# Kernel optimization log

Hardware: AMD Instinct MI355X
Metric: run time of the kernel (lower is better)

Reference implementation:

```python
import jax, jax.numpy as jnp
import numpy as np

B, S, MEM, L, E, H = 8, 512, 512, 4, 512, 8
DH = E // H
OBS = 128
K = MEM + S


def setup_inputs() -> dict:
    key = jax.random.key(0)
    ks = jax.random.split(key, 16)
    def w(k, shape, s=0.02):
        return jax.random.normal(k, shape, jnp.float32) * s
    # causal-with-memory mask: query i may attend to kv positions j <= MEM + i
    mask = jnp.arange(K)[None, None, None, :] <= (MEM + jnp.arange(S))[None, None, :, None]
    return {
        "obs": w(ks[0], (B, S, OBS), 1.0),
        "memories": w(ks[1], (B, MEM, L, E), 1.0),
        "mask": mask,
        "W_enc": w(ks[2], (OBS, E)), "b_enc": jnp.zeros((E,), jnp.float32),
        "ln1_s": jnp.ones((L, E), jnp.float32), "ln1_b": jnp.zeros((L, E), jnp.float32),
        "Wq": w(ks[3], (L, E, H, DH)), "bq": jnp.zeros((L, H, DH), jnp.float32),
        "Wk": w(ks[4], (L, E, H, DH)), "bk": jnp.zeros((L, H, DH), jnp.float32),
        "Wv": w(ks[5], (L, E, H, DH)), "bv": jnp.zeros((L, H, DH), jnp.float32),
        "Wr": w(ks[6], (L, E, H, DH)),
        "u_bias": w(ks[7], (L, H, DH)), "v_bias": w(ks[8], (L, H, DH)),
        "Wo": w(ks[9], (L, H, DH, E)), "bo": jnp.zeros((L, E), jnp.float32),
        "ln2_s": jnp.ones((L, E), jnp.float32), "ln2_b": jnp.zeros((L, E), jnp.float32),
        "W1": w(ks[10], (L, E, E)), "b1": jnp.zeros((L, E), jnp.float32),
        "W2": w(ks[11], (L, E, E)), "b2": jnp.zeros((L, E), jnp.float32),
    }


def _ln(x, s, b, eps=1e-6):
    m = x.mean(-1, keepdims=True)
    v = ((x - m) ** 2).mean(-1, keepdims=True)
    return (x - m) * jax.lax.rsqrt(v + eps) * s + b


def _rel_shift(x):
    # Transformer-XL relative shift: [B,H,Q,Kk] -> shifted [B,H,Q,Kk]
    b, h, q, k = x.shape
    x = jnp.pad(x, ((0, 0), (0, 0), (0, 0), (1, 0)))
    return x.reshape(b, h, k + 1, q)[:, :, 1:, :].reshape(b, h, q, k)


def _forward(obs, memories, mask, W_enc, b_enc, ln1_s, ln1_b, Wq, bq, Wk, bk, Wv, bv,
             Wr, u_bias, v_bias, Wo, bo, ln2_s, ln2_b, W1, b1, W2, b2):
    x = obs @ W_enc + b_enc  # [B,S,E]
    klen = memories.shape[1] + x.shape[1]
    e = x.shape[-1]
    # PositionalEmbedding: pos_seq = [klen, klen-1, ..., 1]
    inv_freq = 1.0 / (10000.0 ** (jnp.arange(0, e, 2, dtype=jnp.float32) / e))
    sin_inp = jnp.outer(jnp.arange(klen, 0, -1, dtype=jnp.float32), inv_freq)
    pe = jnp.concatenate([jnp.sin(sin_inp), jnp.cos(sin_inp)], axis=-1)  # [K,E]
    scale = 1.0 / jnp.sqrt(jnp.asarray(Wq.shape[-1], jnp.float32))
    for i in range(Wq.shape[0]):
        mem_cat = jnp.concatenate([memories[:, :, i], x], axis=1)  # [B,K,E]
        vk = _ln(mem_cat, ln1_s[i], ln1_b[i])
        qn = _ln(x, ln1_s[i], ln1_b[i])
        q = jnp.einsum('bse,ehd->bshd', qn, Wq[i]) + bq[i]
        k = jnp.einsum('bke,ehd->bkhd', vk, Wk[i]) + bk[i]
        vv = jnp.einsum('bke,ehd->bkhd', vk, Wv[i]) + bv[i]
        r = jnp.einsum('ke,ehd->khd', pe, Wr[i])
        ac = jnp.einsum('bqhd,bkhd->bhqk', q + u_bias[i], k)     # content term
        bd = _rel_shift(jnp.einsum('bqhd,khd->bhqk', q + v_bias[i], r))  # position term
        scores = jnp.where(mask, (ac + bd) * scale, jnp.float32(-1e30))
        attn = jax.nn.softmax(scores, axis=-1)
        o = jnp.einsum('bhqk,bkhd->bqhd', attn, vv)
        attn_out = jnp.einsum('bqhd,hde->bqe', o, Wo[i]) + bo[i]
        h = x + attn_out                      # residual (gating=False)
        hn = _ln(h, ln2_s[i], ln2_b[i])
        ff = jax.nn.gelu(hn @ W1[i] + b1[i]) @ W2[i] + b2[i]
        x = ff + h
    return x


def reference(obs, memories, mask, W_enc, b_enc, ln1_s, ln1_b, Wq, bq, Wk, bk, Wv, bv,
              Wr, u_bias, v_bias, Wo, bo, ln2_s, ln2_b, W1, b1, W2, b2):
    return _forward(obs, memories, mask, W_enc, b_enc, ln1_s, ln1_b, Wq, bq, Wk, bk,
                    Wv, bv, Wr, u_bias, v_bias, Wo, bo, ln2_s, ln2_b, W1, b1, W2, b2)
```

## Files before the change

kernel.cpp:

```cpp
#include <hip/hip_runtime.h>
#include <hip/hip_bf16.h>
#include <math.h>

#define B     8
#define S     512
#define MEM   512
#define L     4
#define E     512
#define H     8
#define DH    64
#define OBS   128
#define KLEN  1024
#define FQ    64
#define FK    64

typedef __hip_bfloat16 bf16;
using frag_ab = __attribute__((ext_vector_type(8))) short;
using frag_cd = __attribute__((ext_vector_type(4))) float;

__device__ __forceinline__ float gelu_tanh(float x) {
    return 0.5f * x * (1.0f + tanhf(0.7978845608028654f * (x + 0.044715f * x * x * x)));
}
__device__ __forceinline__ unsigned short f2bs(float x) {
    bf16 h = __float2bfloat16(x); return *(unsigned short*)&h;
}
__device__ __forceinline__ float bs2f(short s) {
    union { unsigned u; float f; } t; t.u = ((unsigned)(unsigned short)s) << 16; return t.f;
}

__global__ __launch_bounds__(256) void setup_kernel(
    const float* __restrict__ obs, bf16* __restrict__ obsb, bf16* __restrict__ pe)
{
    const int i = blockIdx.x * 256 + threadIdx.x;
    if (i < B * S * OBS) {
        obsb[i] = __float2bfloat16(obs[i]);
    } else {
        const int idx = i - B * S * OBS;
        const int p = idx >> 9;
        const int j = idx & 511;
        const float pos = (float)(KLEN - p);
        const int m = (j < 256) ? j : (j - 256);
        const float invf = expf(-(float)(2 * m) * (9.210340371976184f / (float)E));
        const float a = pos * invf;
        pe[idx] = __float2bfloat16((j < 256) ? sinf(a) : cosf(a));
    }
}

__global__ __launch_bounds__(256) void transpose_all_kernel(
    const float* __restrict__ Wq, const float* __restrict__ Wk,
    const float* __restrict__ Wv, const float* __restrict__ Wr,
    const float* __restrict__ Wo, const float* __restrict__ W1,
    const float* __restrict__ W2, const float* __restrict__ Wenc,
    bf16* __restrict__ WqT, bf16* __restrict__ WkvT, bf16* __restrict__ WrT,
    bf16* __restrict__ WoT, bf16* __restrict__ W1T, bf16* __restrict__ W2T,
    bf16* __restrict__ WencT)
{
    __shared__ float t[32][33];
    const int z = blockIdx.z;
    const int bn = blockIdx.x * 32, bk = blockIdx.y * 32;
    const int tx = threadIdx.x & 31, ty = threadIdx.x >> 5;
    if (z == 28) {
        if (blockIdx.y >= OBS / 32) return;
        #pragma unroll
        for (int r = 0; r < 32; r += 8)
            t[ty + r][tx] = Wenc[(size_t)(bk + ty + r) * E + bn + tx];
        __syncthreads();
        #pragma unroll
        for (int r = 0; r < 32; r += 8)
            WencT[(size_t)(bn + ty + r) * OBS + bk + tx] = __float2bfloat16(t[tx][ty + r]);
        return;
    }
    const int which = z >> 2, li = z & 3;
    const size_t so = (size_t)li * E * E;
    const float* src; bf16* dst;
    switch (which) {
        case 0: src = Wq + so; dst = WqT + so; break;
        case 1: src = Wk + so; dst = WkvT + (size_t)li * 2 * E * E; break;
        case 2: src = Wv + so; dst = WkvT + (size_t)li * 2 * E * E + (size_t)E * E; break;
        case 3: src = Wr + so; dst = WrT + so; break;
        case 4: src = Wo + so; dst = WoT + so; break;
        case 5: src = W1 + so; dst = W1T + so; break;
        default: src = W2 + so; dst = W2T + so; break;
    }
    #pragma unroll
    for (int r = 0; r < 32; r += 8)
        t[ty + r][tx] = src[(size_t)(bk + ty + r) * E + bn + tx];
    __syncthreads();
    #pragma unroll
    for (int r = 0; r < 32; r += 8)
        dst[(size_t)(bn + ty + r) * E + bk + tx] = __float2bfloat16(t[tx][ty + r]);
}

__device__ __forceinline__ void gemm_body(
    short* As, short* Bs,
    const bf16* __restrict__ A, const bf16* __restrict__ Bt,
    int m0, int n0, int K, int N,
    const float* bias, const float* bias_u, const float* bias_v,
    const float* res, float* Cf, bf16* Cb, bf16* Cb2, int act, int mode)
{
    const int tid = threadIdx.x;
    const int w = tid >> 6, lane = tid & 63;
    const int wm2 = (w >> 1) * 64, wn2 = (w & 1) * 32;
    const int fr = lane & 15, quad = lane >> 4;

    const int arow = tid >> 1, acol = (tid & 1) * 32;
    const int brow = tid >> 2, bcol = (tid & 3) * 16;
    const short* Ag = (const short*)A + (size_t)(m0 + arow) * K + acol;
    const short* Bg = (const short*)Bt + (size_t)(n0 + brow) * K + bcol;
    short* Asw = &As[arow * 72 + acol];
    short* Bsw = &Bs[brow * 72 + bcol];

    frag_cd acc[4][2];
    #pragma unroll
    for (int i = 0; i < 4; ++i)
        #pragma unroll
        for (int j = 0; j < 2; ++j)
            acc[i][j] = (frag_cd)(0.0f);

    uint4 a0 = *(const uint4*)(Ag);
    uint4 a1 = *(const uint4*)(Ag + 8);
    uint4 a2 = *(const uint4*)(Ag + 16);
    uint4 a3 = *(const uint4*)(Ag + 24);
    uint4 b0 = *(const uint4*)(Bg);
    uint4 b1 = *(const uint4*)(Bg + 8);

    for (int k0 = 0; k0 < K; k0 += 64) {
        __syncthreads();
        *(uint4*)(Asw) = a0; *(uint4*)(Asw + 8) = a1;
        *(uint4*)(Asw + 16) = a2; *(uint4*)(Asw + 24) = a3;
        *(uint4*)(Bsw) = b0; *(uint4*)(Bsw + 8) = b1;
        if (k0 + 64 < K) {
            a0 = *(const uint4*)(Ag + k0 + 64);
            a1 = *(const uint4*)(Ag + k0 + 72);
            a2 = *(const uint4*)(Ag + k0 + 80);
            a3 = *(const uint4*)(Ag + k0 + 88);
            b0 = *(const uint4*)(Bg + k0 + 64);
            b1 = *(const uint4*)(Bg + k0 + 72);
        }
        asm volatile("s_waitcnt lgkmcnt(0)" ::: "memory");
        __builtin_amdgcn_s_barrier();
        __builtin_amdgcn_sched_barrier(0);
        #pragma unroll
        for (int kh = 0; kh < 2; ++kh) {
            frag_ab af[4], bfr[2];
            #pragma unroll
            for (int i = 0; i < 4; ++i)
                af[i] = *(const frag_ab*)&As[(wm2 + i * 16 + fr) * 72 + kh * 32 + quad * 8];
            #pragma unroll
            for (int j = 0; j < 2; ++j)
                bfr[j] = *(const frag_ab*)&Bs[(wn2 + j * 16 + fr) * 72 + kh * 32 + quad * 8];
            #pragma unroll
            for (int i = 0; i < 4; ++i)
                #pragma unroll
                for (int j = 0; j < 2; ++j)
                    acc[i][j] = __builtin_amdgcn_mfma_f32_16x16x32_bf16(af[i], bfr[j], acc[i][j], 0, 0, 0);
        }
    }

    if (mode == 2 && n0 >= 512) {
        short* ts = As;
        __syncthreads();
        #pragma unroll
        for (int i = 0; i < 4; ++i) {
            #pragma unroll
            for (int r = 0; r < 4; ++r) {
                const int kl = wm2 + i * 16 + quad * 4 + r;
                #pragma unroll
                for (int j = 0; j < 2; ++j) {
                    const int dl = wn2 + j * 16 + fr;
                    ts[dl * 130 + kl] =
                        (short)f2bs(acc[i][j][r] + bias_v[(n0 - 512) + dl]);
                }
            }
        }
        __syncthreads();
        const int bb = m0 >> 10;
        const int kb = m0 & 1023;
        const int dl = tid >> 2;
        const int q4 = tid & 3;
        short vals[32];
        #pragma unroll
        for (int i2 = 0; i2 < 32; ++i2) {
            const int kp  = q4 * 32 + i2;
            const int kpl = kp & 63;
            const int src = (kp & 64) + (((kpl & 3) << 4) | (kpl >> 2));
            vals[i2] = ts[dl * 130 + src];
        }
        short* dst = (short*)Cb2 + ((size_t)(bb * E + (n0 - 512) + dl)) * KLEN
                   + kb + q4 * 32;
        *(uint4*)(dst)      = *(const uint4*)&vals[0];
        *(uint4*)(dst + 8)  = *(const uint4*)&vals[8];
        *(uint4*)(dst + 16) = *(const uint4*)&vals[16];
        *(uint4*)(dst + 24) = *(const uint4*)&vals[24];
        return;
    }

    #pragma unroll
    for (int i = 0; i < 4; ++i) {
        #pragma unroll
        for (int r = 0; r < 4; ++r) {
            const int m = m0 + wm2 + i * 16 + quad * 4 + r;
            #pragma unroll
            for (int j = 0; j < 2; ++j) {
                const int n = n0 + wn2 + j * 16 + fr;
                float v = acc[i][j][r];
                if (bias) v += bias[n];
                if (act)  v = gelu_tanh(v);
                if (res)  v += res[(size_t)m * N + n];
                if (mode == 2) {
                    Cb[(size_t)m * 512 + n] = __float2bfloat16(v + bias_u[n]);
                } else if (mode == 1) {
                    Cb[(size_t)m * N + n]  = __float2bfloat16((v + bias_u[n]) * 0.125f);
                    Cb2[(size_t)m * N + n] = __float2bfloat16((v + bias_v[n]) * 0.125f);
                } else {
                    if (Cf) Cf[(size_t)m * N + n] = v;
                    if (Cb) Cb[(size_t)m * N + n] = __float2bfloat16(v);
                }
            }
        }
    }
}

__device__ __forceinline__ void gemm64_body(
    short* As, short* Bs,
    const bf16* __restrict__ A, const bf16* __restrict__ Bt,
    int m0, int n0, int K, int N,
    const float* bias, const float* res, float* Cf, bf16* Cb, int act,
    float* stats)
{
    const int tid = threadIdx.x;
    const int w = tid >> 6, lane = tid & 63;
    const int wm2 = (w >> 1) * 32, wn2 = (w & 1) * 32;
    const int fr = lane & 15, quad = lane >> 4;

    const int arow = tid >> 2, acol = (tid & 3) * 16;
    const short* Ag = (const short*)A + (size_t)(m0 + arow) * K + acol;
    const short* Bg = (const short*)Bt + (size_t)(n0 + arow) * K + acol;
    short* Asw = &As[arow * 72 + acol];
    short* Bsw = &Bs[arow * 72 + acol];

    frag_cd acc[2][2];
    #pragma unroll
    for (int i = 0; i < 2; ++i)
        #pragma unroll
        for (int j = 0; j < 2; ++j)
            acc[i][j] = (frag_cd)(0.0f);

    uint4 a0 = *(const uint4*)(Ag);
    uint4 a1 = *(const uint4*)(Ag + 8);
    uint4 b0 = *(const uint4*)(Bg);
    uint4 b1 = *(const uint4*)(Bg + 8);

    for (int k0 = 0; k0 < K; k0 += 64) {
        __syncthreads();
        *(uint4*)(Asw) = a0; *(uint4*)(Asw + 8) = a1;
        *(uint4*)(Bsw) = b0; *(uint4*)(Bsw + 8) = b1;
        if (k0 + 64 < K) {
            a0 = *(const uint4*)(Ag + k0 + 64);
            a1 = *(const uint4*)(Ag + k0 + 72);
            b0 = *(const uint4*)(Bg + k0 + 64);
            b1 = *(const uint4*)(Bg + k0 + 72);
        }
        asm volatile("s_waitcnt lgkmcnt(0)" ::: "memory");
        __builtin_amdgcn_s_barrier();
        __builtin_amdgcn_sched_barrier(0);
        #pragma unroll
        for (int kh = 0; kh < 2; ++kh) {
            frag_ab af[2], bfr[2];
            #pragma unroll
            for (int i = 0; i < 2; ++i)
                af[i] = *(const frag_ab*)&As[(wm2 + i * 16 + fr) * 72 + kh * 32 + quad * 8];
            #pragma unroll
            for (int j = 0; j < 2; ++j)
                bfr[j] = *(const frag_ab*)&Bs[(wn2 + j * 16 + fr) * 72 + kh * 32 + quad * 8];
            #pragma unroll
            for (int i = 0; i < 2; ++i)
                #pragma unroll
                for (int j = 0; j < 2; ++j)
                    acc[i][j] = __builtin_amdgcn_mfma_f32_16x16x32_bf16(af[i], bfr[j], acc[i][j], 0, 0, 0);
        }
    }

    #pragma unroll
    for (int i = 0; i < 2; ++i) {
        #pragma unroll
        for (int r = 0; r < 4; ++r) {
            const int m = m0 + wm2 + i * 16 + quad * 4 + r;
            float s = 0.0f, sq = 0.0f;
            #pragma unroll
            for (int j = 0; j < 2; ++j) {
                const int n = n0 + wn2 + j * 16 + fr;
                float v = acc[i][j][r];
                if (bias) v += bias[n];
                if (act)  v = gelu_tanh(v);
                if (res)  v += res[(size_t)m * N + n];
                if (Cf) Cf[(size_t)m * N + n] = v;
                if (Cb) Cb[(size_t)m * N + n] = __float2bfloat16(v);
                s += v; sq = fmaf(v, v, sq);
            }
            if (stats) {
                s  += __shfl_xor(s, 1, 64);  sq += __shfl_xor(sq, 1, 64);
                s  += __shfl_xor(s, 2, 64);  sq += __shfl_xor(sq, 2, 64);
                s  += __shfl_xor(s, 4, 64);  sq += __shfl_xor(sq, 4, 64);
                s  += __shfl_xor(s, 8, 64);  sq += __shfl_xor(sq, 8, 64);
                if (fr == 0) {
                    atomicAdd(&stats[2 * m], s);
                    atomicAdd(&stats[2 * m + 1], sq);
                }
            }
        }
    }
}

__global__ __launch_bounds__(256) void mfma_gemm_kernel(
    const bf16* __restrict__ A, const bf16* __restrict__ Bt,
    const float* __restrict__ bias, const float* __restrict__ res,
    float* __restrict__ Cf, bf16* __restrict__ Cb,
    int K, int N, int act, float* stats)
{
    __shared__ short As[64 * 72];
    __shared__ short Bs[64 * 72];
    const int pid = blockIdx.x;
    const int swz = ((pid & 7) << 6) | (pid >> 3);
    gemm64_body(As, Bs, A, Bt, (swz >> 3) * 64, (swz & 7) * 64, K, N,
                bias, res, Cf, Cb, act, stats);
}

__global__ __launch_bounds__(256) void mfma_gemm_ln_kernel(
    const float* __restrict__ A, const bf16* __restrict__ Bt,
    const float* __restrict__ ST,
    const float* __restrict__ gam, const float* __restrict__ bet,
    const float* __restrict__ bias, bf16* __restrict__ Cb)
{
    __shared__ short As[64 * 72];
    __shared__ short Bs[64 * 72];
    __shared__ float gls[E], bls[E];
    const int pid = blockIdx.x;
    const int swz = ((pid & 7) << 6) | (pid >> 3);
    const int m0 = (swz >> 3) * 64, n0 = (swz & 7) * 64;
    const int tid = threadIdx.x;
    *(float2*)&gls[tid * 2] = *(const float2*)&gam[tid * 2];
    *(float2*)&bls[tid * 2] = *(const float2*)&bet[tid * 2];

    const int w = tid >> 6, lane = tid & 63;
    const int wm2 = (w >> 1) * 32, wn2 = (w & 1) * 32;
    const int fr = lane & 15, quad = lane >> 4;

    const int arow = tid >> 2, acol = (tid & 3) * 16;
    const int g = m0 + arow;
    const float mean = ST[2 * g] * (1.0f / E);
    const float var  = ST[2 * g + 1] * (1.0f / E) - mean * mean;
    const float rstd = rsqrtf(var + 1e-6f);
    const float* Agf = A + (size_t)g * E + acol;
    const short* Bg = (const short*)Bt + (size_t)(n0 + arow) * E + acol;
    short* Asw = &As[arow * 72 + acol];
    short* Bsw = &Bs[arow * 72 + acol];

    frag_cd acc[2][2];
    #pragma unroll
    for (int i = 0; i < 2; ++i)
        #pragma unroll
        for (int j = 0; j < 2; ++j)
            acc[i][j] = (frag_cd)(0.0f);

    float4 f0 = *(const float4*)(Agf);
    float4 f1 = *(const float4*)(Agf + 4);
    float4 f2 = *(const float4*)(Agf + 8);
    float4 f3 = *(const float4*)(Agf + 12);
    uint4 b0 = *(const uint4*)(Bg);
    uint4 b1 = *(const uint4*)(Bg + 8);

    for (int k0 = 0; k0 < E; k0 += 64) {
        __syncthreads();
        {
            const float* gp = &gls[k0 + acol];
            const float* bp = &bls[k0 + acol];
            union { uint4 u; unsigned short s[8]; } p0, p1;
            p0.s[0] = f2bs((f0.x - mean) * rstd * gp[0]  + bp[0]);
            p0.s[1] = f2bs((f0.y - mean) * rstd * gp[1]  + bp[1]);
            p0.s[2] = f2bs((f0.z - mean) * rstd * gp[2]  + bp[2]);
            p0.s[3] = f2bs((f0.w - mean) * rstd * gp[3]  + bp[3]);
            p0.s[4] = f2bs((f1.x - mean) * rstd * gp[4]  + bp[4]);
            p0.s[5] = f2bs((f1.y - mean) * rstd * gp[5]  + bp[5]);
            p0.s[6] = f2bs((f1.z - mean) * rstd * gp[6]  + bp[6]);
            p0.s[7] = f2bs((f1.w - mean) * rstd * gp[7]  + bp[7]);
            p1.s[0] = f2bs((f2.x - mean) * rstd * gp[8]  + bp[8]);
            p1.s[1] = f2bs((f2.y - mean) * rstd * gp[9]  + bp[9]);
            p1.s[2] = f2bs((f2.z - mean) * rstd * gp[10] + bp[10]);
            p1.s[3] = f2bs((f2.w - mean) * rstd * gp[11] + bp[11]);
            p1.s[4] = f2bs((f3.x - mean) * rstd * gp[12] + bp[12]);
            p1.s[5] = f2bs((f3.y - mean) * rstd * gp[13] + bp[13]);
            p1.s[6] = f2bs((f3.z - mean) * rstd * gp[14] + bp[14]);
            p1.s[7] = f2bs((f3.w - mean) * rstd * gp[15] + bp[15]);
            *(uint4*)(Asw) = p0.u; *(uint4*)(Asw + 8) = p1.u;
        }
        *(uint4*)(Bsw) = b0; *(uint4*)(Bsw + 8) = b1;
        if (k0 + 64 < E) {
            f0 = *(const float4*)(Agf + k0 + 64);
            f1 = *(const float4*)(Agf + k0 + 68);
            f2 = *(const float4*)(Agf + k0 + 72);
            f3 = *(const float4*)(Agf + k0 + 76);
            b0 = *(const uint4*)(Bg + k0 + 64);
            b1 = *(const uint4*)(Bg + k0 + 72);
        }
        asm volatile("s_waitcnt lgkmcnt(0)" ::: "memory");
        __builtin_amdgcn_s_barrier();
        __builtin_amdgcn_sched_barrier(0);
        #pragma unroll
        for (int kh = 0; kh < 2; ++kh) {
            frag_ab af[2], bfr[2];
            #pragma unroll
            for (int i = 0; i < 2; ++i)
                af[i] = *(const frag_ab*)&As[(wm2 + i * 16 + fr) * 72 + kh * 32 + quad * 8];
            #pragma unroll
            for (int j = 0; j < 2; ++j)
                bfr[j] = *(const frag_ab*)&Bs[(wn2 + j * 16 + fr) * 72 + kh * 32 + quad * 8];
            #pragma unroll
            for (int i = 0; i < 2; ++i)
                #pragma unroll
                for (int j = 0; j < 2; ++j)
                    acc[i][j] = __builtin_amdgcn_mfma_f32_16x16x32_bf16(af[i], bfr[j], acc[i][j], 0, 0, 0);
        }
    }

    #pragma unroll
    for (int i = 0; i < 2; ++i) {
        #pragma unroll
        for (int r = 0; r < 4; ++r) {
            const int m = m0 + wm2 + i * 16 + quad * 4 + r;
            #pragma unroll
            for (int j = 0; j < 2; ++j) {
                const int n = n0 + wn2 + j * 16 + fr;
                const float v = gelu_tanh(acc[i][j][r] + bias[n]);
                Cb[(size_t)m * E + n] = __float2bfloat16(v);
            }
        }
    }
}

__global__ __launch_bounds__(256) void qkvr_kernel(
    const bf16* __restrict__ QN, const bf16* __restrict__ VK,
    const bf16* __restrict__ PE_, const bf16* __restrict__ WqT,
    const bf16* __restrict__ WkvT, const bf16* __restrict__ WrT,
    const float* __restrict__ bq, const float* __restrict__ ub,
    const float* __restrict__ vbias, const float* __restrict__ bk,
    const float* __restrict__ bv,
    bf16* __restrict__ QU, bf16* __restrict__ QV,
    bf16* __restrict__ KB, bf16* __restrict__ VT, bf16* __restrict__ RB)
{
    __shared__ short As[128 * 72];
    __shared__ short Bs[64 * 72];
    const int bid = blockIdx.x;
    if (bid < 256) {
        const int swz = ((bid & 7) << 5) | (bid >> 3);
        gemm_body(As, Bs, QN, WqT, (swz >> 3) * 128, (swz & 7) * 64, E, E,
                  bq, ub, vbias, nullptr, nullptr, QU, QV, 0, 1);
    } else if (bid < 1280) {
        const int id = bid - 256;
        const int swz = ((id & 7) << 7) | (id >> 3);
        gemm_body(As, Bs, VK, WkvT, (swz >> 4) * 128, (swz & 15) * 64, E, 2 * E,
                  nullptr, bk, bv, nullptr, nullptr, KB, VT, 0, 2);
    } else {
        const int id = bid - 1280;
        const int swz = ((id & 7) << 3) | (id >> 3);
        gemm_body(As, Bs, PE_, WrT, (swz >> 3) * 128, (swz & 7) * 64, E, E,
                  nullptr, nullptr, nullptr, nullptr, nullptr, RB, nullptr, 0, 0);
    }
}

__global__ __launch_bounds__(256) void ln1_kernel(
    const float* __restrict__ mem, const float* __restrict__ X, int li,
    const float* __restrict__ gam, const float* __restrict__ bet,
    bf16* __restrict__ qn, bf16* __restrict__ vkdst, float* __restrict__ st)
{
    const int blk = blockIdx.x;
    const int t = threadIdx.x;
    if (blk < 32) st[blk * 256 + t] = 0.0f;
    const bool isMem = blk < B * MEM;
    const int rr = isMem ? blk : (blk - B * MEM);
    const float* sp = isMem ? (mem + ((size_t)rr * L + li) * E)
                            : (X + (size_t)rr * E);
    const float x0 = sp[t], x1 = sp[t + 256];
    float s = x0 + x1, ss = fmaf(x0, x0, x1 * x1);
    #pragma unroll
    for (int off = 32; off; off >>= 1) { s += __shfl_down(s, off, 64); ss += __shfl_down(ss, off, 64); }
    __shared__ float tmp[8];
    const int wid = t >> 6, lane = t & 63;
    if (!lane) { tmp[wid] = s; tmp[4 + wid] = ss; }
    __syncthreads();
    s = tmp[0] + tmp[1] + tmp[2] + tmp[3];
    ss = tmp[4] + tmp[5] + tmp[6] + tmp[7];
    const float mean = s * (1.0f / E);
    const float var = ss * (1.0f / E) - mean * mean;
    const float rstd = rsqrtf(var + 1e-6f);
    const float y0 = (x0 - mean) * rstd * gam[t] + bet[t];
    const float y1 = (x1 - mean) * rstd * gam[t + 256] + bet[t + 256];
    const int b = rr >> 9, p = rr & 511;
    if (isMem) {
        bf16* dst = vkdst + ((size_t)b * KLEN + p) * E;
        dst[t] = __float2bfloat16(y0); dst[t + 256] = __float2bfloat16(y1);
    } else {
        qn[(size_t)rr * E + t]       = __float2bfloat16(y0);
        qn[(size_t)rr * E + t + 256] = __float2bfloat16(y1);
        bf16* d2 = vkdst + ((size_t)b * KLEN + MEM + p) * E;
        d2[t] = __float2bfloat16(y0); d2[t + 256] = __float2bfloat16(y1);
    }
}

__global__ __launch_bounds__(256) void mfma_flash_kernel(
    const bf16* __restrict__ Qu,
    const bf16* __restrict__ Qv,
    const bf16* __restrict__ Kb,
    const bf16* __restrict__ Vt,
    const bf16* __restrict__ Rb,
    bf16* __restrict__ O)
{
    const int pid = blockIdx.x;
    const int swz = ((pid & 7) << 6) | (pid >> 3);
    const int qphys = swz & 7;
    const int hb = swz >> 3;
    const int h = hb & 7, b = hb >> 3;
    const int qt = (qphys & 1) ? (7 - (qphys >> 1)) : (qphys >> 1);
    const int q0 = qt * FQ;
    const int t = threadIdx.x;
    const int w = t >> 6, lane = t & 63;
    const int fr = lane & 15, quad = lane >> 4;
    const int qbase = q0 + w * 16;

    __shared__ short Ks[64 * 64];
    __shared__ short Vs[64 * 64];
    __shared__ short Rs[128 * 64];
    __shared__ short BDs[4 * 80 * 18];
    __shared__ short Ps[4 * 16 * 64];

    const int fxk = fr & 7;
    const int xq0 = (quad ^ fxk) << 3;
    const int xq1 = ((quad + 4) ^ fxk) << 3;

    const short* quptr = (const short*)Qu + ((size_t)(b * S + qbase + fr)) * E + h * DH + quad * 8;
    const frag_ab au0 = *(const frag_ab*)(quptr);
    const frag_ab au1 = *(const frag_ab*)(quptr + 32);
    const short* qvptr = (const short*)Qv + ((size_t)(b * S + qbase + fr)) * E + h * DH + quad * 8;
    const frag_ab av0 = *(const frag_ab*)(qvptr);
    const frag_ab av1 = *(const frag_ab*)(qvptr + 32);

    frag_cd accO[4];
    #pragma unroll
    for (int i = 0; i < 4; ++i) accO[i] = (frag_cd)(0.0f);
    float mrow[4] = {-3.0e38f, -3.0e38f, -3.0e38f, -3.0e38f};
    float lrow[4] = {0.f, 0.f, 0.f, 0.f};

    const int srow = t >> 2, scol = (t & 3) * 16;
    const short* kg = (const short*)Kb + ((size_t)(b * KLEN + srow)) * E + h * DH + scol;
    const short* vg = (const short*)Vt + ((size_t)(b * E + h * DH + srow)) * KLEN + scol;
    const int sxs = srow & 7;
    const int scb = (t & 3) * 2;
    const int kvw0 = (srow << 6) + (((scb    ) ^ sxs) << 3);
    const int kvw1 = (srow << 6) + (((scb + 1) ^ sxs) << 3);
    const int ntb0 = 3 - w;
    const int b0 = 448 - q0;

    {
        const int rr = t >> 1, rc = (t & 1) * 32;
        const int j = b0 + rr;
        const int slot = j & 127;
        const int sx = slot & 7, cb = rc >> 3;
        const short* rp = (const short*)Rb + (size_t)j * E + h * DH + rc;
        *(uint4*)&Rs[(slot << 6) + (((cb    ) ^ sx) << 3)] = *(const uint4*)(rp);
        *(uint4*)&Rs[(slot << 6) + (((cb + 1) ^ sx) << 3)] = *(const uint4*)(rp + 8);
        *(uint4*)&Rs[(slot << 6) + (((cb + 2) ^ sx) << 3)] = *(const uint4*)(rp + 16);
        *(uint4*)&Rs[(slot << 6) + (((cb + 3) ^ sx) << 3)] = *(const uint4*)(rp + 24);
    }

    const int ntiles = 9 + qt;

    const int r64 = t >> 2, rc4 = (t & 3) * 16;
    uint4 ka0, ka1, va0, va1, ra0, ra1;
    int rslot = 0;
    {
        ka0 = *(const uint4*)(kg);
        ka1 = *(const uint4*)(kg + 8);
        va0 = *(const uint4*)(vg);
        va1 = *(const uint4*)(vg + 8);
    }

    for (int kt = 0; kt < ntiles; ++kt) {
        const int k0 = kt * FK;
        __syncthreads();
        {
            *(uint4*)&Ks[kvw0] = ka0;
            *(uint4*)&Ks[kvw1] = ka1;
            *(uint4*)&Vs[kvw0] = va0;
            *(uint4*)&Vs[kvw1] = va1;
        }
        if (kt >= 1) {
            const int sx = rslot & 7;
            *(uint4*)&Rs[(rslot << 6) + (((scb    ) ^ sx) << 3)] = ra0;
            *(uint4*)&Rs[(rslot << 6) + (((scb + 1) ^ sx) << 3)] = ra1;
        }
        if (kt + 1 < ntiles) {
            const short* kp = kg + (size_t)(k0 + FK) * E;
            ka0 = *(const uint4*)(kp);
            ka1 = *(const uint4*)(kp + 8);
            const short* vp = vg + k0 + FK;
            va0 = *(const uint4*)(vp);
            va1 = *(const uint4*)(vp + 8);
            int j = b0 + 64 * (kt + 1) + 64 + r64;
            rslot = j & 127;
            if (j > KLEN - 1) j = KLEN - 1;
            const short* rp = (const short*)Rb + (size_t)j * E + h * DH + rc4;
            ra0 = *(const uint4*)(rp);
            ra1 = *(const uint4*)(rp + 8);
        }
        asm volatile("s_waitcnt lgkmcnt(0)" ::: "memory");
        __builtin_amdgcn_s_barrier();
        __builtin_amdgcn_sched_barrier(0);

        const int roff = (b0 + 64 * kt) & 127;

        __builtin_amdgcn_s_setprio(1);
        #pragma unroll
        for (int i = 0; i < 5; ++i) {
            const int ntb = ntb0 + i;
            const int slot = (roff + ntb * 16 + fr) & 127;
            const frag_ab rf0 = *(const frag_ab*)&Rs[(slot << 6) + xq0];
            const frag_ab rf1 = *(const frag_ab*)&Rs[(slot << 6) + xq1];
            frag_cd z = (frag_cd)(0.0f);
            z = __builtin_amdgcn_mfma_f32_16x16x32_bf16(av0, rf0, z, 0, 0, 0);
            z = __builtin_amdgcn_mfma_f32_16x16x32_bf16(av1, rf1, z, 0, 0, 0);
            union { unsigned u[2]; unsigned short sh[4]; } pk;
            pk.sh[0] = f2bs(z[0]); pk.sh[1] = f2bs(z[1]);
            pk.sh[2] = f2bs(z[2]); pk.sh[3] = f2bs(z[3]);
            const int bdw = (w * 80 + i * 16 + fr) * 18 + quad * 4;
            *(unsigned*)&BDs[bdw]     = pk.u[0];
            *(unsigned*)&BDs[bdw + 2] = pk.u[1];
        }

        frag_cd sc[4];
        #pragma unroll
        for (int nt = 0; nt < 4; ++nt) {
            const int krow = (nt * 16 + fr) << 6;
            const frag_ab kf0 = *(const frag_ab*)&Ks[krow + xq0];
            const frag_ab kf1 = *(const frag_ab*)&Ks[krow + xq1];
            frag_cd z = (frag_cd)(0.0f);
            z = __builtin_amdgcn_mfma_f32_16x16x32_bf16(au0, kf0, z, 0, 0, 0);
            z = __builtin_amdgcn_mfma_f32_16x16x32_bf16(au1, kf1, z, 0, 0, 0);
            sc[nt] = z;
        }
        __builtin_amdgcn_s_setprio(0);

        const bool edge = (kt == ntiles - 1);
        #pragma unroll
        for (int r = 0; r < 4; ++r) {
            const int qw = quad * 4 + r;
            float sv[4];
            #pragma unroll
            for (int nt = 0; nt < 4; ++nt) {
                const int jlr = nt * 16 + fr + 15 - qw;
                const float bd = bs2f(BDs[(w * 80 + jlr) * 18 + qw]);
                sv[nt] = sc[nt][r] + bd;
            }
            if (edge) {
                const int qrow = qbase + qw;
                #pragma unroll
                for (int nt = 0; nt < 4; ++nt)
                    if (k0 + nt * 16 + fr > MEM + qrow) sv[nt] = -1e30f;
            }
            const float locmax = fmaxf(fmaxf(sv[0], sv[1]), fmaxf(sv[2], sv[3]));
            if (__any(locmax > mrow[r] + 4.0f)) {
                float tm = locmax;
                tm = fmaxf(tm, __shfl_xor(tm, 1, 64));
                tm = fmaxf(tm, __shfl_xor(tm, 2, 64));
                tm = fmaxf(tm, __shfl_xor(tm, 4, 64));
                tm = fmaxf(tm, __shfl_xor(tm, 8, 64));
                const float mn = fmaxf(mrow[r], tm);
                const float al = __expf(mrow[r] - mn);
                lrow[r] *= al;
                #pragma unroll
                for (int nt = 0; nt < 4; ++nt) accO[nt][r] *= al;
                mrow[r] = mn;
            }
            const float p0 = __expf(sv[0] - mrow[r]), p1 = __expf(sv[1] - mrow[r]);
            const float p2 = __expf(sv[2] - mrow[r]), p3 = __expf(sv[3] - mrow[r]);
            lrow[r] += (p0 + p1) + (p2 + p3);
            union { uint2 u2; unsigned short sh[4]; } pq;
            pq.sh[0] = f2bs(p0); pq.sh[1] = f2bs(p1);
            pq.sh[2] = f2bs(p2); pq.sh[3] = f2bs(p3);
            const int pw = (w << 10) + (qw << 6)
                         + (((fr >> 1) ^ (qw & 7)) << 3) + ((fr & 1) << 2);
            *(uint2*)&Ps[pw] = pq.u2;
        }

        const frag_ab pf0 = *(const frag_ab*)&Ps[(w << 10) + (fr << 6) + xq0];
        const frag_ab pf1 = *(const frag_ab*)&Ps[(w << 10) + (fr << 6) + xq1];
        __builtin_amdgcn_s_setprio(1);
        #pragma unroll
        for (int nt = 0; nt < 4; ++nt) {
            const int vrow = (nt * 16 + fr) << 6;
            const frag_ab vf0 = *(const frag_ab*)&Vs[vrow + xq0];
            const frag_ab vf1 = *(const frag_ab*)&Vs[vrow + xq1];
            accO[nt] = __builtin_amdgcn_mfma_f32_16x16x32_bf16(pf0, vf0, accO[nt], 0, 0, 0);
            accO[nt] = __builtin_amdgcn_mfma_f32_16x16x32_bf16(pf1, vf1, accO[nt], 0, 0, 0);
        }
        __builtin_amdgcn_s_setprio(0);
    }

    #pragma unroll
    for (int r = 0; r < 4; ++r) {
        float lsum = lrow[r];
        lsum += __shfl_xor(lsum, 1, 64);
        lsum += __shfl_xor(lsum, 2, 64);
        lsum += __shfl_xor(lsum, 4, 64);
        lsum += __shfl_xor(lsum, 8, 64);
        const float inv = 1.0f / lsum;
        bf16* po = O + ((size_t)(b * S + qbase + quad * 4 + r)) * E + h * DH + fr;
        #pragma unroll
        for (int nt = 0; nt < 4; ++nt)
            po[nt * 16] = __float2bfloat16(accO[nt][r] * inv);
    }
}

extern "C" void kernel_launch(void* const* d_in, const int* in_sizes, int n_in,
                              void* d_out, int out_size, void* d_ws, size_t ws_size,
                              hipStream_t stream)
{
    const float* obs  = (const float*)d_in[0];
    const float* mem  = (const float*)d_in[1];
    const float* Wenc = (const float*)d_in[3];
    const float* benc = (const float*)d_in[4];
    const float* ln1s = (const float*)d_in[5];
    const float* ln1b = (const float*)d_in[6];
    const float* Wq   = (const float*)d_in[7];
    const float* bq   = (const float*)d_in[8];
    const float* Wk   = (const float*)d_in[9];
    const float* bk   = (const float*)d_in[10];
    const float* Wv   = (const float*)d_in[11];
    const float* bv   = (const float*)d_in[12];
    const float* Wr   = (const float*)d_in[13];
    const float* ub   = (const float*)d_in[14];
    const float* vb   = (const float*)d_in[15];
    const float* Wo   = (const float*)d_in[16];
    const float* bo   = (const float*)d_in[17];
    const float* ln2s = (const float*)d_in[18];
    const float* ln2b = (const float*)d_in[19];
    const float* W1   = (const float*)d_in[20];
    const float* b1   = (const float*)d_in[21];
    const float* W2   = (const float*)d_in[22];
    const float* b2   = (const float*)d_in[23];

    float* wsf = (float*)d_ws;
    float* X = wsf;
    bf16* wsb = (bf16*)(wsf + (size_t)B * S * E);
    size_t ob = 0;
    bf16* OBSb = wsb + ob; ob += (size_t)B * S * OBS;
    bf16* QNb  = wsb + ob; ob += (size_t)B * S * E;
    bf16* PEb  = wsb + ob; ob += (size_t)KLEN * E;
    bf16* RBb  = wsb + ob; ob += (size_t)KLEN * E;
    bf16* WencT= wsb + ob; ob += (size_t)OBS * E;
    bf16* WqT  = wsb + ob; ob += (size_t)L * E * E;
    bf16* WkvT = wsb + ob; ob += (size_t)L * 2 * E * E;
    bf16* WrT  = wsb + ob; ob += (size_t)L * E * E;
    bf16* WoT  = wsb + ob; ob += (size_t)L * E * E;
    bf16* W1T  = wsb + ob; ob += (size_t)L * E * E;
    bf16* W2T  = wsb + ob; ob += (size_t)L * E * E;
    bf16* QUb  = wsb + ob; ob += (size_t)B * S * E;
    bf16* QVb  = wsb + ob; ob += (size_t)B * S * E;
    bf16* KBb  = wsb + ob; ob += (size_t)B * KLEN * E;
    bf16* VTb  = wsb + ob; ob += (size_t)B * E * KLEN;
    bf16* OBb  = wsb + ob; ob += (size_t)B * S * E;
    float* ST  = (float*)(wsb + ob); ob += 16384;
    char* uni = (char*)(wsb + ob);
    bf16*  VKb = (bf16*)uni;
    float* HB  = (float*)uni;
    bf16*  FFb = (bf16*)(uni + ((size_t)8 << 20));


    transpose_all_kernel<<<dim3(E / 32, E / 32, 29), 256, 0, stream>>>(
        Wq, Wk, Wv, Wr, Wo, W1, W2, Wenc, WqT, WkvT, WrT, WoT, W1T, W2T, WencT);
    setup_kernel<<<(B * S * OBS + KLEN * E) / 256, 256, 0, stream>>>(obs, OBSb, PEb);

    mfma_gemm_kernel<<<512, 256, 0, stream>>>(
        OBSb, WencT, benc, nullptr, X, nullptr, OBS, E, 0, nullptr);

    for (int li = 0; li < L; ++li) {
        const size_t wOff = (size_t)li * E * E;
        const size_t vOff = (size_t)li * E;

        ln1_kernel<<<2 * B * S, 256, 0, stream>>>(
            mem, X, li, ln1s + vOff, ln1b + vOff, QNb, VKb, ST);

        qkvr_kernel<<<1344, 256, 0, stream>>>(
            QNb, VKb, PEb, WqT + wOff, WkvT + (size_t)li * 2 * E * E, WrT + wOff,
            bq + vOff, ub + vOff, vb + vOff, bk + vOff, bv + vOff,
            QUb, QVb, KBb, VTb, RBb);

        mfma_flash_kernel<<<512, 256, 0, stream>>>(
            QUb, QVb, KBb, VTb, RBb, OBb);

        mfma_gemm_kernel<<<512, 256, 0, stream>>>(
            OBb, WoT + wOff, bo + vOff, X, HB, nullptr, E, E, 0, ST);
        mfma_gemm_ln_kernel<<<512, 256, 0, stream>>>(
            HB, W1T + wOff, ST, ln2s + vOff, ln2b + vOff, b1 + vOff, FFb);
        float* dst = (li == L - 1) ? (float*)d_out : X;
        mfma_gemm_kernel<<<512, 256, 0, stream>>>(
            FFb, W2T + wOff, b2 + vOff, HB, dst, nullptr, E, E, 0, nullptr);
    }
}
```

Before: 580.9 us.

## Fuse LayerNorm-1 into QKV projection GEMM prologue using precomputed row stats

Removes the per-layer ln1 kernel. Q/K/V GEMMs now read fp32 X and memory rows directly and normalize them in the A-tile load path. Row sum and sum-of-squares for X are accumulated in the preceding GEMM epilogues, and those for the memories are computed once up front by a new memstats kernel. This saves a kernel launch and the bf16 round trip of the normalized activations, at the cost of doubled fp32 A-tile reads and extra ALU work in the GEMM prologue. It also relies on epilogue stat accumulation into STx and on zeroing that buffer inside the flash kernel.

```diff
diff --git a/kernel.cpp b/kernel.cpp
--- a/kernel.cpp
+++ b/kernel.cpp
@@ -29,9 +29,11 @@
 }
 
 __global__ __launch_bounds__(256) void setup_kernel(
-    const float* __restrict__ obs, bf16* __restrict__ obsb, bf16* __restrict__ pe)
+    const float* __restrict__ obs, bf16* __restrict__ obsb, bf16* __restrict__ pe,
+    float* __restrict__ stx)
 {
     const int i = blockIdx.x * 256 + threadIdx.x;
+    if (blockIdx.x < 32) stx[i] = 0.0f;
     if (i < B * S * OBS) {
         obsb[i] = __float2bfloat16(obs[i]);
     } else {
@@ -46,6 +48,26 @@
     }
 }
 
+__global__ __launch_bounds__(256) void memstats_kernel(
+    const float* __restrict__ mem, float* __restrict__ stm)
+{
+    const int rid = blockIdx.x;
+    const int t = threadIdx.x;
+    const float* sp = mem + (size_t)rid * E;
+    const float x0 = sp[t], x1 = sp[t + 256];
+    float s = x0 + x1, ss = fmaf(x0, x0, x1 * x1);
+    #pragma unroll
+    for (int off = 32; off; off >>= 1) { s += __shfl_down(s, off, 64); ss += __shfl_down(ss, off, 64); }
+    __shared__ float tmp[8];
+    const int wid = t >> 6, lane = t & 63;
+    if (!lane) { tmp[wid] = s; tmp[4 + wid] = ss; }
+    __syncthreads();
+    if (t == 0) {
+        stm[2 * rid]     = tmp[0] + tmp[1] + tmp[2] + tmp[3];
+        stm[2 * rid + 1] = tmp[4] + tmp[5] + tmp[6] + tmp[7];
+    }
+}
+
 __global__ __launch_bounds__(256) void transpose_all_kernel(
     const float* __restrict__ Wq, const float* __restrict__ Wk,
     const float* __restrict__ Wv, const float* __restrict__ Wr,
@@ -94,9 +116,7 @@
 __device__ __forceinline__ void gemm_body(
     short* As, short* Bs,
     const bf16* __restrict__ A, const bf16* __restrict__ Bt,
-    int m0, int n0, int K, int N,
-    const float* bias, const float* bias_u, const float* bias_v,
-    const float* res, float* Cf, bf16* Cb, bf16* Cb2, int act, int mode)
+    int m0, int n0, int K, int N, bf16* Cb)
 {
     const int tid = threadIdx.x;
     const int w = tid >> 6, lane = tid & 63;
@@ -157,6 +177,137 @@
         }
     }
 
+    #pragma unroll
+    for (int i = 0; i < 4; ++i)
+        #pragma unroll
+        for (int r = 0; r < 4; ++r) {
+            const int m = m0 + wm2 + i * 16 + quad * 4 + r;
+            #pragma unroll
+            for (int j = 0; j < 2; ++j) {
+                const int n = n0 + wn2 + j * 16 + fr;
+                Cb[(size_t)m * N + n] = __float2bfloat16(acc[i][j][r]);
+            }
+        }
+}
+
+__device__ __forceinline__ void gemm_body_lnA(
+    short* As, short* Bs, const float* gls, const float* bls,
+    const float* __restrict__ A0, size_t rowStride,
+    const float* __restrict__ ST0, int stStride,
+    const bf16* __restrict__ Bt,
+    int m0, int n0, int N,
+    const float* bias, const float* bias_u, const float* bias_v,
+    bf16* Cb, bf16* Cb2, int mode)
+{
+    const int tid = threadIdx.x;
+    const int w = tid >> 6, lane = tid & 63;
+    const int wm2 = (w >> 1) * 64, wn2 = (w & 1) * 32;
+    const int fr = lane & 15, quad = lane >> 4;
+
+    const int arow = tid >> 1, acol = (tid & 1) * 32;
+    const int brow = tid >> 2, bcol = (tid & 3) * 16;
+    const float* Ag = A0 + (size_t)arow * rowStride + acol;
+    const short* Bg = (const short*)Bt + (size_t)(n0 + brow) * E + bcol;
+    short* Asw = &As[arow * 72 + acol];
+    short* Bsw = &Bs[brow * 72 + bcol];
+
+    const float* st = ST0 + arow * stStride;
+    const float mean = st[0] * (1.0f / E);
+    const float var  = st[1] * (1.0f / E) - mean * mean;
+    const float rstd = rsqrtf(var + 1e-6f);
+
+    frag_cd acc[4][2];
+    #pragma unroll
+    for (int i = 0; i < 4; ++i)
+        #pragma unroll
+        for (int j = 0; j < 2; ++j)
+            acc[i][j] = (frag_cd)(0.0f);
+
+    float4 f0 = *(const float4*)(Ag);
+    float4 f1 = *(const float4*)(Ag + 4);
+    float4 f2 = *(const float4*)(Ag + 8);
+    float4 f3 = *(const float4*)(Ag + 12);
+    float4 f4 = *(const float4*)(Ag + 16);
+    float4 f5 = *(const float4*)(Ag + 20);
+    float4 f6 = *(const float4*)(Ag + 24);
+    float4 f7 = *(const float4*)(Ag + 28);
+    uint4 b0 = *(const uint4*)(Bg);
+    uint4 b1 = *(const uint4*)(Bg + 8);
+
+    for (int k0 = 0; k0 < E; k0 += 64) {
+        __syncthreads();
+        {
+            const float* gp = &gls[k0 + acol];
+            const float* bp = &bls[k0 + acol];
+            union { uint4 u; unsigned short s[8]; } p0, p1, p2, p3;
+            p0.s[0] = f2bs((f0.x - mean) * rstd * gp[0]  + bp[0]);
+            p0.s[1] = f2bs((f0.y - mean) * rstd * gp[1]  + bp[1]);
+            p0.s[2] = f2bs((f0.z - mean) * rstd * gp[2]  + bp[2]);
+            p0.s[3] = f2bs((f0.w - mean) * rstd * gp[3]  + bp[3]);
+            p0.s[4] = f2bs((f1.x - mean) * rstd * gp[4]  + bp[4]);
+            p0.s[5] = f2bs((f1.y - mean) * rstd * gp[5]  + bp[5]);
+            p0.s[6] = f2bs((f1.z - mean) * rstd * gp[6]  + bp[6]);
+            p0.s[7] = f2bs((f1.w - mean) * rstd * gp[7]  + bp[7]);
+            p1.s[0] = f2bs((f2.x - mean) * rstd * gp[8]  + bp[8]);
+            p1.s[1] = f2bs((f2.y - mean) * rstd * gp[9]  + bp[9]);
+            p1.s[2] = f2bs((f2.z - mean) * rstd * gp[10] + bp[10]);
+            p1.s[3] = f2bs((f2.w - mean) * rstd * gp[11] + bp[11]);
+            p1.s[4] = f2bs((f3.x - mean) * rstd * gp[12] + bp[12]);
+            p1.s[5] = f2bs((f3.y - mean) * rstd * gp[13] + bp[13]);
+            p1.s[6] = f2bs((f3.z - mean) * rstd * gp[14] + bp[14]);
+            p1.s[7] = f2bs((f3.w - mean) * rstd * gp[15] + bp[15]);
+            p2.s[0] = f2bs((f4.x - mean) * rstd * gp[16] + bp[16]);
+            p2.s[1] = f2bs((f4.y - mean) * rstd * gp[17] + bp[17]);
+            p2.s[2] = f2bs((f4.z - mean) * rstd * gp[18] + bp[18]);
+            p2.s[3] = f2bs((f4.w - mean) * rstd * gp[19] + bp[19]);
+            p2.s[4] = f2bs((f5.x - mean) * rstd * gp[20] + bp[20]);
+            p2.s[5] = f2bs((f5.y - mean) * rstd * gp[21] + bp[21]);
+            p2.s[6] = f2bs((f5.z - mean) * rstd * gp[22] + bp[22]);
+            p2.s[7] = f2bs((f5.w - mean) * rstd * gp[23] + bp[23]);
+            p3.s[0] = f2bs((f6.x - mean) * rstd * gp[24] + bp[24]);
+            p3.s[1] = f2bs((f6.y - mean) * rstd * gp[25] + bp[25]);
+            p3.s[2] = f2bs((f6.z - mean) * rstd * gp[26] + bp[26]);
+            p3.s[3] = f2bs((f6.w - mean) * rstd * gp[27] + bp[27]);
+            p3.s[4] = f2bs((f7.x - mean) * rstd * gp[28] + bp[28]);
+            p3.s[5] = f2bs((f7.y - mean) * rstd * gp[29] + bp[29]);
+            p3.s[6] = f2bs((f7.z - mean) * rstd * gp[30] + bp[30]);
+            p3.s[7] = f2bs((f7.w - mean) * rstd * gp[31] + bp[31]);
+            *(uint4*)(Asw) = p0.u; *(uint4*)(Asw + 8) = p1.u;
+            *(uint4*)(Asw + 16) = p2.u; *(uint4*)(Asw + 24) = p3.u;
+        }
+        *(uint4*)(Bsw) = b0; *(uint4*)(Bsw + 8) = b1;
+        if (k0 + 64 < E) {
+            f0 = *(const float4*)(Ag + k0 + 64);
+            f1 = *(const float4*)(Ag + k0 + 68);
+            f2 = *(const float4*)(Ag + k0 + 72);
+            f3 = *(const float4*)(Ag + k0 + 76);
+            f4 = *(const float4*)(Ag + k0 + 80);
+            f5 = *(const float4*)(Ag + k0 + 84);
+            f6 = *(const float4*)(Ag + k0 + 88);
+            f7 = *(const float4*)(Ag + k0 + 92);
+            b0 = *(const uint4*)(Bg + k0 + 64);
+            b1 = *(const uint4*)(Bg + k0 + 72);
+        }
+        asm volatile("s_waitcnt lgkmcnt(0)" ::: "memory");
+        __builtin_amdgcn_s_barrier();
+        __builtin_amdgcn_sched_barrier(0);
+        #pragma unroll
+        for (int kh = 0; kh < 2; ++kh) {
+            frag_ab af[4], bfr[2];
+            #pragma unroll
+            for (int i = 0; i < 4; ++i)
+                af[i] = *(const frag_ab*)&As[(wm2 + i * 16 + fr) * 72 + kh * 32 + quad * 8];
+            #pragma unroll
+            for (int j = 0; j < 2; ++j)
+                bfr[j] = *(const frag_ab*)&Bs[(wn2 + j * 16 + fr) * 72 + kh * 32 + quad * 8];
+            #pragma unroll
+            for (int i = 0; i < 4; ++i)
+                #pragma unroll
+                for (int j = 0; j < 2; ++j)
+                    acc[i][j] = __builtin_amdgcn_mfma_f32_16x16x32_bf16(af[i], bfr[j], acc[i][j], 0, 0, 0);
+        }
+    }
+
     if (mode == 2 && n0 >= 512) {
         short* ts = As;
         __syncthreads();
@@ -204,17 +355,12 @@
             for (int j = 0; j < 2; ++j) {
                 const int n = n0 + wn2 + j * 16 + fr;
                 float v = acc[i][j][r];
-                if (bias) v += bias[n];
-                if (act)  v = gelu_tanh(v);
-                if (res)  v += res[(size_t)m * N + n];
                 if (mode == 2) {
                     Cb[(size_t)m * 512 + n] = __float2bfloat16(v + bias_u[n]);
-                } else if (mode == 1) {
+                } else {
+                    v += bias[n];
                     Cb[(size_t)m * N + n]  = __float2bfloat16((v + bias_u[n]) * 0.125f);
                     Cb2[(size_t)m * N + n] = __float2bfloat16((v + bias_v[n]) * 0.125f);
-                } else {
-                    if (Cf) Cf[(size_t)m * N + n] = v;
-                    if (Cb) Cb[(size_t)m * N + n] = __float2bfloat16(v);
                 }
             }
         }
@@ -424,7 +570,7 @@
     }
 
     #pragma unroll
-    for (int i = 0; i < 2; ++i) {
+    for (int i = 0; i < 2; ++i)
         #pragma unroll
         for (int r = 0; r < 4; ++r) {
             const int m = m0 + wm2 + i * 16 + quad * 4 + r;
@@ -435,11 +581,12 @@
                 Cb[(size_t)m * E + n] = __float2bfloat16(v);
             }
         }
-    }
 }
 
 __global__ __launch_bounds__(256) void qkvr_kernel(
-    const bf16* __restrict__ QN, const bf16* __restrict__ VK,
+    const float* __restrict__ X, const float* __restrict__ mem, int li,
+    const float* __restrict__ STx, const float* __restrict__ STM,
+    const float* __restrict__ gam, const float* __restrict__ bet,
     const bf16* __restrict__ PE_, const bf16* __restrict__ WqT,
     const bf16* __restrict__ WkvT, const bf16* __restrict__ WrT,
     const float* __restrict__ bq, const float* __restrict__ ub,
@@ -450,72 +597,51 @@
 {
     __shared__ short As[128 * 72];
     __shared__ short Bs[64 * 72];
+    __shared__ float gls[E], bls[E];
     const int bid = blockIdx.x;
+    const int tid = threadIdx.x;
+    if (bid < 1280) {
+        *(float2*)&gls[tid * 2] = *(const float2*)&gam[tid * 2];
+        *(float2*)&bls[tid * 2] = *(const float2*)&bet[tid * 2];
+    }
     if (bid < 256) {
         const int swz = ((bid & 7) << 5) | (bid >> 3);
-        gemm_body(As, Bs, QN, WqT, (swz >> 3) * 128, (swz & 7) * 64, E, E,
-                  bq, ub, vbias, nullptr, nullptr, QU, QV, 0, 1);
+        const int m0 = (swz >> 3) * 128, n0 = (swz & 7) * 64;
+        gemm_body_lnA(As, Bs, gls, bls,
+                      X + (size_t)m0 * E, E, STx + (size_t)m0 * 2, 2,
+                      WqT, m0, n0, E, bq, ub, vbias, QU, QV, 1);
     } else if (bid < 1280) {
         const int id = bid - 256;
         const int swz = ((id & 7) << 7) | (id >> 3);
-        gemm_body(As, Bs, VK, WkvT, (swz >> 4) * 128, (swz & 15) * 64, E, 2 * E,
-                  nullptr, bk, bv, nullptr, nullptr, KB, VT, 0, 2);
+        const int m0 = (swz >> 4) * 128, n0 = (swz & 15) * 64;
+        const int bb = m0 >> 10, local = m0 & 1023;
+        if (local < 512) {
+            const size_t rid0 = ((size_t)bb * 512 + local) * L + li;
+            gemm_body_lnA(As, Bs, gls, bls,
+                          mem + rid0 * E, (size_t)L * E, STM + rid0 * 2, 2 * L,
+                          WkvT, m0, n0, 2 * E, nullptr, bk, bv, KB, VT, 2);
+        } else {
+            const int g0 = bb * 512 + (local - 512);
+            gemm_body_lnA(As, Bs, gls, bls,
+                          X + (size_t)g0 * E, E, STx + (size_t)g0 * 2, 2,
+                          WkvT, m0, n0, 2 * E, nullptr, bk, bv, KB, VT, 2);
+        }
     } else {
         const int id = bid - 1280;
         const int swz = ((id & 7) << 3) | (id >> 3);
-        gemm_body(As, Bs, PE_, WrT, (swz >> 3) * 128, (swz & 7) * 64, E, E,
-                  nullptr, nullptr, nullptr, nullptr, nullptr, RB, nullptr, 0, 0);
-    }
-}
-
-__global__ __launch_bounds__(256) void ln1_kernel(
-    const float* __restrict__ mem, const float* __restrict__ X, int li,
-    const float* __restrict__ gam, const float* __restrict__ bet,
-    bf16* __restrict__ qn, bf16* __restrict__ vkdst, float* __restrict__ st)
-{
-    const int blk = blockIdx.x;
-    const int t = threadIdx.x;
-    if (blk < 32) st[blk * 256 + t] = 0.0f;
-    const bool isMem = blk < B * MEM;
-    const int rr = isMem ? blk : (blk - B * MEM);
-    const float* sp = isMem ? (mem + ((size_t)rr * L + li) * E)
-                            : (X + (size_t)rr * E);
-    const float x0 = sp[t], x1 = sp[t + 256];
-    float s = x0 + x1, ss = fmaf(x0, x0, x1 * x1);
-    #pragma unroll
-    for (int off = 32; off; off >>= 1) { s += __shfl_down(s, off, 64); ss += __shfl_down(ss, off, 64); }
-    __shared__ float tmp[8];
-    const int wid = t >> 6, lane = t & 63;
-    if (!lane) { tmp[wid] = s; tmp[4 + wid] = ss; }
-    __syncthreads();
-    s = tmp[0] + tmp[1] + tmp[2] + tmp[3];
-    ss = tmp[4] + tmp[5] + tmp[6] + tmp[7];
-    const float mean = s * (1.0f / E);
-    const float var = ss * (1.0f / E) - mean * mean;
-    const float rstd = rsqrtf(var + 1e-6f);
-    const float y0 = (x0 - mean) * rstd * gam[t] + bet[t];
-    const float y1 = (x1 - mean) * rstd * gam[t + 256] + bet[t + 256];
-    const int b = rr >> 9, p = rr & 511;
-    if (isMem) {
-        bf16* dst = vkdst + ((size_t)b * KLEN + p) * E;
-        dst[t] = __float2bfloat16(y0); dst[t + 256] = __float2bfloat16(y1);
-    } else {
-        qn[(size_t)rr * E + t]       = __float2bfloat16(y0);
-        qn[(size_t)rr * E + t + 256] = __float2bfloat16(y1);
-        bf16* d2 = vkdst + ((size_t)b * KLEN + MEM + p) * E;
-        d2[t] = __float2bfloat16(y0); d2[t + 256] = __float2bfloat16(y1);
+        gemm_body(As, Bs, PE_, WrT, (swz >> 3) * 128, (swz & 7) * 64, E, E, RB);
     }
 }
 
 __global__ __launch_bounds__(256) void mfma_flash_kernel(
-    const bf16* __restrict__ Qu,
-    const bf16* __restrict__ Qv,
-    const bf16* __restrict__ Kb,
-    const bf16* __restrict__ Vt,
-    const bf16* __restrict__ Rb,
-    bf16* __restrict__ O)
+    const bf16* __restrict__ Qu, const bf16* __restrict__ Qv,
+    const bf16* __restrict__ Kb, const bf16* __restrict__ Vt,
+    const bf16* __restrict__ Rb, bf16* __restrict__ O,
+    float* __restrict__ st2, float* __restrict__ stx)
 {
     const int pid = blockIdx.x;
+    if (pid < 32) st2[pid * 256 + threadIdx.x] = 0.0f;
+    else if (pid < 64) stx[(pid - 32) * 256 + threadIdx.x] = 0.0f;
     const int swz = ((pid & 7) << 6) | (pid >> 3);
     const int qphys = swz & 7;
     const int hb = swz >> 3;
@@ -753,7 +879,6 @@
     bf16* wsb = (bf16*)(wsf + (size_t)B * S * E);
     size_t ob = 0;
     bf16* OBSb = wsb + ob; ob += (size_t)B * S * OBS;
-    bf16* QNb  = wsb + ob; ob += (size_t)B * S * E;
     bf16* PEb  = wsb + ob; ob += (size_t)KLEN * E;
     bf16* RBb  = wsb + ob; ob += (size_t)KLEN * E;
     bf16* WencT= wsb + ob; ob += (size_t)OBS * E;
@@ -768,41 +893,41 @@
     bf16* KBb  = wsb + ob; ob += (size_t)B * KLEN * E;
     bf16* VTb  = wsb + ob; ob += (size_t)B * E * KLEN;
     bf16* OBb  = wsb + ob; ob += (size_t)B * S * E;
-    float* ST  = (float*)(wsb + ob); ob += 16384;
+    float* ST2 = (float*)(wsb + ob); ob += 16384;
+    float* STx = (float*)(wsb + ob); ob += 16384;
+    float* STM = (float*)(wsb + ob); ob += 131072;
     char* uni = (char*)(wsb + ob);
-    bf16*  VKb = (bf16*)uni;
     float* HB  = (float*)uni;
     bf16*  FFb = (bf16*)(uni + ((size_t)8 << 20));
 
-
     transpose_all_kernel<<<dim3(E / 32, E / 32, 29), 256, 0, stream>>>(
         Wq, Wk, Wv, Wr, Wo, W1, W2, Wenc, WqT, WkvT, WrT, WoT, W1T, W2T, WencT);
-    setup_kernel<<<(B * S * OBS + KLEN * E) / 256, 256, 0, stream>>>(obs, OBSb, PEb);
+    setup_kernel<<<(B * S * OBS + KLEN * E) / 256, 256, 0, stream>>>(
+        obs, OBSb, PEb, STx);
+    memstats_kernel<<<B * MEM * L, 256, 0, stream>>>(mem, STM);
 
     mfma_gemm_kernel<<<512, 256, 0, stream>>>(
-        OBSb, WencT, benc, nullptr, X, nullptr, OBS, E, 0, nullptr);
+        OBSb, WencT, benc, nullptr, X, nullptr, OBS, E, 0, STx);
 
     for (int li = 0; li < L; ++li) {
         const size_t wOff = (size_t)li * E * E;
         const size_t vOff = (size_t)li * E;
 
-        ln1_kernel<<<2 * B * S, 256, 0, stream>>>(
-            mem, X, li, ln1s + vOff, ln1b + vOff, QNb, VKb, ST);
-
         qkvr_kernel<<<1344, 256, 0, stream>>>(
-            QNb, VKb, PEb, WqT + wOff, WkvT + (size_t)li * 2 * E * E, WrT + wOff,
+            X, mem, li, STx, STM, ln1s + vOff, ln1b + vOff,
+            PEb, WqT + wOff, WkvT + (size_t)li * 2 * E * E, WrT + wOff,
             bq + vOff, ub + vOff, vb + vOff, bk + vOff, bv + vOff,
             QUb, QVb, KBb, VTb, RBb);
 
         mfma_flash_kernel<<<512, 256, 0, stream>>>(
-            QUb, QVb, KBb, VTb, RBb, OBb);
+            QUb, QVb, KBb, VTb, RBb, OBb, ST2, STx);
 
         mfma_gemm_kernel<<<512, 256, 0, stream>>>(
-            OBb, WoT + wOff, bo + vOff, X, HB, nullptr, E, E, 0, ST);
+            OBb, WoT + wOff, bo + vOff, X, HB, nullptr, E, E, 0, ST2);
         mfma_gemm_ln_kernel<<<512, 256, 0, stream>>>(
-            HB, W1T + wOff, ST, ln2s + vOff, ln2b + vOff, b1 + vOff, FFb);
+            HB, W1T + wOff, ST2, ln2s + vOff, ln2b + vOff, b1 + vOff, FFb);
         float* dst = (li == L - 1) ? (float*)d_out : X;
         mfma_gemm_kernel<<<512, 256, 0, stream>>>(
-            FFb, W2T + wOff, b2 + vOff, HB, dst, nullptr, E, E, 0, nullptr);
-    }
-}
+            FFb, W2T + wOff, b2 + vOff, HB, dst, nullptr, E, E, 0, STx);
+    }
+}
```

Result: slower. 677.5 us (+16.6%).
